# Optimization experiments

Hardware: AMD Instinct MI355X
Metric: run time of the kernel (lower is better)

Reference implementation:

```python
import jax, jax.numpy as jnp
import numpy as np

B, T, N, D = 2, 16, 512, 256
HID, HEADS = 256, 8
HD = HID // HEADS // 2  # 16
SCALE = HD ** -0.5
LAMBDA_INIT = 0.8 - 0.6 * float(np.exp(-0.3 * (2 - 1)))  # layer_idx = 2
LN_EPS = 1e-5


def setup_inputs() -> dict:
    key = jax.random.key(0)
    ks = jax.random.split(key, 8)
    return {
        "x": jax.random.normal(ks[0], (B, T, N, D), dtype=jnp.float32),
        "Wq": jax.random.normal(ks[1], (D, HID), dtype=jnp.float32) * (D ** -0.5),
        "Wk": jax.random.normal(ks[2], (D, HID), dtype=jnp.float32) * (D ** -0.5),
        "Wv": jax.random.normal(ks[3], (D, HID), dtype=jnp.float32) * (D ** -0.5),
        "lq1": jax.random.normal(ks[4], (HD,), dtype=jnp.float32) * 0.1,
        "lk1": jax.random.normal(ks[5], (HD,), dtype=jnp.float32) * 0.1,
        "lq2": jax.random.normal(ks[6], (HD,), dtype=jnp.float32) * 0.1,
        "lk2": jax.random.normal(ks[7], (HD,), dtype=jnp.float32) * 0.1,
        "ln_gamma": jnp.ones((2 * HD,), dtype=jnp.float32),
        "ln_beta": jnp.zeros((2 * HD,), dtype=jnp.float32),
    }


def _attn_pair(q, k, v1, v2):
    # q,k,v*: [BT, N, H, HD]; shared softmax applied to both value halves
    p = jax.nn.softmax(jnp.einsum('bnhd,bmhd->bhnm', q, k) * SCALE, axis=-1)
    o1 = jnp.einsum('bhnm,bmhd->bnhd', p, v1)
    o2 = jnp.einsum('bhnm,bmhd->bnhd', p, v2)
    return jnp.concatenate([o1, o2], axis=-1)  # [BT, N, H, 2*HD]


def reference(x, Wq, Wk, Wv, lq1, lk1, lq2, lk2, ln_gamma, ln_beta):
    b, t, n, d = x.shape
    # 1x1 Conv2d over channel dim == per-token linear projection
    q = jnp.einsum('btnd,dh->btnh', x, Wq).reshape(b * t, n, HEADS, 2 * HD)
    k = jnp.einsum('btnd,dh->btnh', x, Wk).reshape(b * t, n, HEADS, 2 * HD)
    v = jnp.einsum('btnd,dh->btnh', x, Wv).reshape(b * t, n, HEADS, 2 * HD)
    q1, q2 = jnp.split(q, 2, axis=-1)
    k1, k2 = jnp.split(k, 2, axis=-1)
    v1, v2 = jnp.split(v, 2, axis=-1)
    attn1 = _attn_pair(q1, k1, v1, v2)
    attn2 = _attn_pair(q2, k2, v1, v2)
    lam = jnp.exp(jnp.sum(lq1 * lk1)) - jnp.exp(jnp.sum(lq2 * lk2)) + LAMBDA_INIT
    y = attn1 - lam * attn2  # [BT, N, H, 2*HD]
    mu = jnp.mean(y, axis=-1, keepdims=True)
    var = jnp.mean(jnp.square(y - mu), axis=-1, keepdims=True)
    y = (y - mu) * jax.lax.rsqrt(var + LN_EPS) * ln_gamma + ln_beta
    y = y * (1.0 - LAMBDA_INIT)
    return y.reshape(b, t, n, HEADS * 2 * HD)
```

## Files before the change

### kernel.cpp

```cpp
#include <hip/hip_runtime.h>
#include <cmath>

typedef unsigned short u16;
typedef unsigned int   u32;
typedef __attribute__((ext_vector_type(8))) short short8;
typedef __attribute__((ext_vector_type(4))) float f32x4;

constexpr int BT    = 32;
constexpr int NTOK  = 512;
constexpr int DIM   = 256;
constexpr int HID   = 256;
constexpr int M_ROWS = BT * NTOK;
constexpr int HM     = M_ROWS * 32;
constexpr size_t TENS = (size_t)M_ROWS * HID;
constexpr float LAMBDA_INIT  = 0.35550906759096927f;
constexpr float ONE_MINUS_LI = 0.6444909324090307f;
constexpr float LN_EPS = 1e-5f;
constexpr float QSCALE = 0.36067376022224085f;

#define MFMA16(a, b, c) __builtin_amdgcn_mfma_f32_16x16x32_bf16((a), (b), (c), 0, 0, 0)

__device__ __forceinline__ u16 f2bf(float f) {
    u32 u = __float_as_uint(f);
    return (u16)((u + 0x7FFFu + ((u >> 16) & 1u)) >> 16);
}

__device__ __forceinline__ float fexp2(float x) {
#if defined(__has_builtin) && __has_builtin(__builtin_amdgcn_exp2f)
    return __builtin_amdgcn_exp2f(x);
#else
    return exp2f(x);
#endif
}

__device__ __forceinline__ u32 pack_bf16(float a, float b) {
    u32 ua = __float_as_uint(a) + 0x8000u;
    u32 ub = __float_as_uint(b) + 0x8000u;
    return __builtin_amdgcn_perm(ub, ua, 0x07060302u);
}

__global__ __launch_bounds__(256) void prep_w(const float* __restrict__ Wq,
                                              const float* __restrict__ Wk,
                                              const float* __restrict__ Wv,
                                              u16* __restrict__ Wt) {
    const float* W = (blockIdx.z == 0) ? Wq : (blockIdx.z == 1) ? Wk : Wv;
    u16* dst = Wt + (size_t)blockIdx.z * 65536;
    __shared__ float T[64][65];
    const int k0 = blockIdx.x * 64, n0 = blockIdx.y * 64;
    const int tr = threadIdx.x >> 4;
    const int tc = threadIdx.x & 15;
    #pragma unroll
    for (int i = 0; i < 4; ++i) {
        int row = tr + i * 16;
        float4 v = *(const float4*)&W[(size_t)(k0 + row) * HID + n0 + tc * 4];
        T[row][tc * 4 + 0] = v.x; T[row][tc * 4 + 1] = v.y;
        T[row][tc * 4 + 2] = v.z; T[row][tc * 4 + 3] = v.w;
    }
    __syncthreads();
    #pragma unroll
    for (int i = 0; i < 4; ++i) {
        int n = tr + i * 16;
        int k4 = tc * 4;
        uint2 pk;
        pk.x = (u32)f2bf(T[k4 + 0][n]) | ((u32)f2bf(T[k4 + 1][n]) << 16);
        pk.y = (u32)f2bf(T[k4 + 2][n]) | ((u32)f2bf(T[k4 + 3][n]) << 16);
        *(uint2*)&dst[(size_t)(n0 + n) * DIM + k0 + k4] = pk;
    }
}

__global__ __launch_bounds__(256, 3) void proj_kernel(
    const float* __restrict__ x, const u16* __restrict__ Wt,
    u16* __restrict__ Qh, u16* __restrict__ Kh, u16* __restrict__ Vh)
{
    __shared__ u16 As[64 * 72];
    __shared__ u16 Bs[3][64 * 72];

    const int tid  = threadIdx.x;
    const int m0   = blockIdx.x * 64;
    const int n0   = blockIdx.y * 64;
    const int lane = tid & 63;
    const int wv   = tid >> 6;
    const int q16  = lane & 15;
    const int quad = lane >> 4;
    const int mw   = (wv >> 1) * 32;
    const int nw   = (wv & 1) * 32;

    const int sr = tid >> 2;
    const int sc = (tid & 3) * 16;

    f32x4 acc[3][4];
    #pragma unroll
    for (int z = 0; z < 3; ++z)
        #pragma unroll
        for (int t = 0; t < 4; ++t)
            acc[z][t] = (f32x4){0.f, 0.f, 0.f, 0.f};

    for (int kk = 0; kk < DIM; kk += 64) {
        {
            const float4* xs = (const float4*)&x[(size_t)(m0 + sr) * DIM + kk + sc];
            float4 g0 = xs[0], g1 = xs[1], g2 = xs[2], g3 = xs[3];
            uint4 o0, o1;
            o0.x = (u32)f2bf(g0.x) | ((u32)f2bf(g0.y) << 16);
            o0.y = (u32)f2bf(g0.z) | ((u32)f2bf(g0.w) << 16);
            o0.z = (u32)f2bf(g1.x) | ((u32)f2bf(g1.y) << 16);
            o0.w = (u32)f2bf(g1.z) | ((u32)f2bf(g1.w) << 16);
            o1.x = (u32)f2bf(g2.x) | ((u32)f2bf(g2.y) << 16);
            o1.y = (u32)f2bf(g2.z) | ((u32)f2bf(g2.w) << 16);
            o1.z = (u32)f2bf(g3.x) | ((u32)f2bf(g3.y) << 16);
            o1.w = (u32)f2bf(g3.z) | ((u32)f2bf(g3.w) << 16);
            *(uint4*)&As[sr * 72 + sc]     = o0;
            *(uint4*)&As[sr * 72 + sc + 8] = o1;
        }
        #pragma unroll
        for (int z = 0; z < 3; ++z) {
            const uint4* ws4 = (const uint4*)&Wt[(size_t)z * 65536 + (size_t)(n0 + sr) * DIM + kk + sc];
            *(uint4*)&Bs[z][sr * 72 + sc]     = ws4[0];
            *(uint4*)&Bs[z][sr * 72 + sc + 8] = ws4[1];
        }
        __syncthreads();
        #pragma unroll
        for (int kc = 0; kc < 2; ++kc) {
            short8 a0 = *(const short8*)&As[(mw +      q16) * 72 + kc * 32 + quad * 8];
            short8 a1 = *(const short8*)&As[(mw + 16 + q16) * 72 + kc * 32 + quad * 8];
            #pragma unroll
            for (int z = 0; z < 3; ++z) {
                short8 b0 = *(const short8*)&Bs[z][(nw +      q16) * 72 + kc * 32 + quad * 8];
                short8 b1 = *(const short8*)&Bs[z][(nw + 16 + q16) * 72 + kc * 32 + quad * 8];
                acc[z][0] = MFMA16(a0, b0, acc[z][0]);
                acc[z][1] = MFMA16(a0, b1, acc[z][1]);
                acc[z][2] = MFMA16(a1, b0, acc[z][2]);
                acc[z][3] = MFMA16(a1, b1, acc[z][3]);
            }
        }
        __syncthreads();
    }

    const int hcol = (n0 + nw) >> 5;
    #pragma unroll
    for (int z = 0; z < 3; ++z) {
        u16* C = (z == 0) ? Qh : (z == 1) ? Kh : Vh;
        u16* base = C + (size_t)hcol * HM;
        const float s = (z == 0) ? QSCALE : 1.0f;
        #pragma unroll
        for (int r = 0; r < 4; ++r) {
            const int row = m0 + mw + quad * 4 + r;
            base[(size_t)row * 32 + q16]             = f2bf(acc[z][0][r] * s);
            base[(size_t)row * 32 + q16 + 16]        = f2bf(acc[z][1][r] * s);
            base[(size_t)(row + 16) * 32 + q16]      = f2bf(acc[z][2][r] * s);
            base[(size_t)(row + 16) * 32 + q16 + 16] = f2bf(acc[z][3][r] * s);
        }
    }
}

__global__ __launch_bounds__(256, 3) void attn_kernel(
    const u16* __restrict__ Qh, const u16* __restrict__ Kh, const u16* __restrict__ Vh,
    const float* __restrict__ lq1, const float* __restrict__ lk1,
    const float* __restrict__ lq2, const float* __restrict__ lk2,
    const float* __restrict__ gamma, const float* __restrict__ beta,
    float* __restrict__ out)
{
    __shared__ u16 Ks[256 * 40];
    __shared__ u16 Vts[32 * 264];
    __shared__ u16 Pbuf[4][2][16 * 40];

    const int qh  = blockIdx.x;
    const int h   = blockIdx.y;
    const int bt  = blockIdx.z;
    const int tid = threadIdx.x;
    const int lane = tid & 63;
    const int wv   = tid >> 6;
    const int q16  = lane & 15;
    const int quad = lane >> 4;

    float sa = 0.f, sb = 0.f;
    #pragma unroll
    for (int d = 0; d < 16; ++d) { sa += lq1[d] * lk1[d]; sb += lq2[d] * lk2[d]; }
    const float lam = __expf(sa) - __expf(sb) + LAMBDA_INIT;

    short8 qv[2];
    #pragma unroll
    for (int qbi = 0; qbi < 2; ++qbi) {
        const int qrow = bt * NTOK + qh * 128 + (qbi * 4 + wv) * 16 + q16;
        qv[qbi] = *(const short8*)(Qh + (size_t)h * HM + (size_t)qrow * 32 + quad * 8);
    }

    const short8 z8 = {0, 0, 0, 0, 0, 0, 0, 0};
    const f32x4  z4 = {0.f, 0.f, 0.f, 0.f};

    f32x4 o1lo[2], o1hi[2], o2lo[2], o2hi[2];
    #pragma unroll
    for (int qbi = 0; qbi < 2; ++qbi) {
        o1lo[qbi] = z4; o1hi[qbi] = z4; o2lo[qbi] = z4; o2hi[qbi] = z4;
    }
    float l1[2] = {0.f, 0.f}, l2[2] = {0.f, 0.f};

    u16* P1 = &Pbuf[wv][0][0];
    u16* P2 = &Pbuf[wv][1][0];

    for (int chunk = 0; chunk < 2; ++chunk) {
        if (chunk) __syncthreads();
        {
            const uint4* src = (const uint4*)(Kh + (size_t)h * HM +
                                (size_t)(bt * NTOK + chunk * 256 + tid) * 32);
            uint4* dst = (uint4*)&Ks[tid * 40];
            dst[0] = src[0]; dst[1] = src[1]; dst[2] = src[2]; dst[3] = src[3];
        }
        if (tid < 128) {
            const int j0 = tid * 2;
            const u16* v0 = Vh + (size_t)h * HM + (size_t)(bt * NTOK + chunk * 256 + j0) * 32;
            union U { uint4 q[4]; u32 w[16]; } ra, rb;
            #pragma unroll
            for (int i = 0; i < 4; ++i) {
                ra.q[i] = ((const uint4*)v0)[i];
                rb.q[i] = ((const uint4*)(v0 + 32))[i];
            }
            #pragma unroll
            for (int w = 0; w < 16; ++w) {
                u32 lo = __builtin_amdgcn_perm(rb.w[w], ra.w[w], 0x05040100u);
                u32 hi = __builtin_amdgcn_perm(rb.w[w], ra.w[w], 0x07060302u);
                *(u32*)&Vts[(2 * w)     * 264 + j0] = lo;
                *(u32*)&Vts[(2 * w + 1) * 264 + j0] = hi;
            }
        }
        __syncthreads();

        #pragma unroll
        for (int qbi = 0; qbi < 2; ++qbi) {
            const short8 A1 = (lane < 32) ? qv[qbi] : z8;
            const short8 A2 = (lane < 32) ? z8 : qv[qbi];
            for (int kc = 0; kc < 8; ++kc) {
                #pragma unroll
                for (int sub = 0; sub < 2; ++sub) {
                    const int key0 = kc * 32 + sub * 16;
                    short8 kf = *(const short8*)&Ks[(key0 + q16) * 40 + quad * 8];
                    f32x4 s1 = MFMA16(kf, A1, z4);
                    f32x4 s2 = MFMA16(kf, A2, z4);
                    float p0 = fexp2(s1[0]), p1 = fexp2(s1[1]);
                    float p2 = fexp2(s1[2]), p3 = fexp2(s1[3]);
                    l1[qbi] += (p0 + p1) + (p2 + p3);
                    uint2 w1; w1.x = pack_bf16(p0, p1); w1.y = pack_bf16(p2, p3);
                    *(uint2*)&P1[q16 * 40 + sub * 16 + quad * 4] = w1;
                    float r0 = fexp2(s2[0]), r1 = fexp2(s2[1]);
                    float r2 = fexp2(s2[2]), r3 = fexp2(s2[3]);
                    l2[qbi] += (r0 + r1) + (r2 + r3);
                    uint2 w2; w2.x = pack_bf16(r0, r1); w2.y = pack_bf16(r2, r3);
                    *(uint2*)&P2[q16 * 40 + sub * 16 + quad * 4] = w2;
                }
                short8 pf1 = *(const short8*)&P1[q16 * 40 + quad * 8];
                short8 pf2 = *(const short8*)&P2[q16 * 40 + quad * 8];
                short8 vlo = *(const short8*)&Vts[q16        * 264 + kc * 32 + quad * 8];
                short8 vhi = *(const short8*)&Vts[(16 + q16) * 264 + kc * 32 + quad * 8];
                o1lo[qbi] = MFMA16(pf1, vlo, o1lo[qbi]);
                o1hi[qbi] = MFMA16(pf1, vhi, o1hi[qbi]);
                o2lo[qbi] = MFMA16(pf2, vlo, o2lo[qbi]);
                o2hi[qbi] = MFMA16(pf2, vhi, o2hi[qbi]);
            }
        }
    }

    const float g_lo = gamma[q16],      g_hi = gamma[16 + q16];
    const float b_lo = beta[q16],       b_hi = beta[16 + q16];

    #pragma unroll
    for (int qbi = 0; qbi < 2; ++qbi) {
        float a = l1[qbi], b = l2[qbi];
        a += __shfl_xor(a, 16); a += __shfl_xor(a, 32);
        b += __shfl_xor(b, 16); b += __shfl_xor(b, 32);
        const float inv1 = 1.0f / a;
        const float inv2 = 1.0f / b;
        #pragma unroll
        for (int r = 0; r < 4; ++r) {
            const float i1 = __shfl(inv1, quad * 4 + r);
            const float i2 = __shfl(inv2, quad * 4 + r);
            const float ylo = o1lo[qbi][r] * i1 - lam * (o2lo[qbi][r] * i2);
            const float yhi = o1hi[qbi][r] * i1 - lam * (o2hi[qbi][r] * i2);

            float s  = ylo + yhi;
            float s2 = ylo * ylo + yhi * yhi;
            #pragma unroll
            for (int off = 1; off < 16; off <<= 1) {
                s  += __shfl_xor(s,  off);
                s2 += __shfl_xor(s2, off);
            }
            const float mu   = s * (1.0f / 32.0f);
            const float var  = s2 * (1.0f / 32.0f) - mu * mu;
            const float rstd = rsqrtf(var + LN_EPS);

            const int row = bt * NTOK + qh * 128 + (qbi * 4 + wv) * 16 + quad * 4 + r;
            float* orow = out + (size_t)row * HID + h * 32;
            orow[q16]      = ((ylo - mu) * rstd * g_lo + b_lo) * ONE_MINUS_LI;
            orow[16 + q16] = ((yhi - mu) * rstd * g_hi + b_hi) * ONE_MINUS_LI;
        }
    }
}

extern "C" void kernel_launch(void* const* d_in, const int* in_sizes, int n_in,
                              void* d_out, int out_size, void* d_ws, size_t ws_size,
                              hipStream_t stream) {
    const float* x   = (const float*)d_in[0];
    const float* Wq  = (const float*)d_in[1];
    const float* Wk  = (const float*)d_in[2];
    const float* Wv  = (const float*)d_in[3];
    const float* lq1 = (const float*)d_in[4];
    const float* lk1 = (const float*)d_in[5];
    const float* lq2 = (const float*)d_in[6];
    const float* lk2 = (const float*)d_in[7];
    const float* gam = (const float*)d_in[8];
    const float* bet = (const float*)d_in[9];
    float* out = (float*)d_out;

    u16* ws = (u16*)d_ws;
    u16* Wt = ws;
    u16* Qh = Wt + 3 * 65536;
    u16* Kh = Qh + TENS;
    u16* Vh = Kh + TENS;

    hipLaunchKernelGGL(prep_w, dim3(4, 4, 3), dim3(256), 0, stream, Wq, Wk, Wv, Wt);
    hipLaunchKernelGGL(proj_kernel, dim3(M_ROWS / 64, HID / 64), dim3(256), 0, stream,
                       x, Wt, Qh, Kh, Vh);
    hipLaunchKernelGGL(attn_kernel, dim3(4, 8, 32), dim3(256), 0, stream,
                       Qh, Kh, Vh, lq1, lk1, lq2, lk2, gam, bet, out);
}
```

Baseline: 134.3 us.

## Fuse QKV projection into attention kernel with per-(bt,head) blocks

Merges the projection and attention kernels into one kernel with one 512-thread block per (batch-time, head). Each block recomputes its head's Q/K/V from x using 32x32 MFMAs and keeps the first half of K/V in shared memory, spilling the rest to a small scratch. This removes the global round trip of the full Q/K/V tensors and one launch. In exchange x is re-read by every head (8x), the grid is only 256 blocks, and the bf16 packing now truncates instead of rounding.

```diff
diff --git a/kernel.cpp b/kernel.cpp
--- a/kernel.cpp
+++ b/kernel.cpp
@@ -3,22 +3,21 @@
 
 typedef unsigned short u16;
 typedef unsigned int   u32;
-typedef __attribute__((ext_vector_type(8))) short short8;
-typedef __attribute__((ext_vector_type(4))) float f32x4;
+typedef __attribute__((ext_vector_type(8)))  short short8;
+typedef __attribute__((ext_vector_type(4)))  float f32x4;
+typedef __attribute__((ext_vector_type(16))) float f32x16;
 
 constexpr int BT    = 32;
 constexpr int NTOK  = 512;
 constexpr int DIM   = 256;
 constexpr int HID   = 256;
-constexpr int M_ROWS = BT * NTOK;
-constexpr int HM     = M_ROWS * 32;
-constexpr size_t TENS = (size_t)M_ROWS * HID;
 constexpr float LAMBDA_INIT  = 0.35550906759096927f;
 constexpr float ONE_MINUS_LI = 0.6444909324090307f;
 constexpr float LN_EPS = 1e-5f;
 constexpr float QSCALE = 0.36067376022224085f;
 
 #define MFMA16(a, b, c) __builtin_amdgcn_mfma_f32_16x16x32_bf16((a), (b), (c), 0, 0, 0)
+#define MFMA32(a, b, c) __builtin_amdgcn_mfma_f32_32x32x16_bf16((a), (b), (c), 0, 0, 0)
 
 __device__ __forceinline__ u16 f2bf(float f) {
     u32 u = __float_as_uint(f);
@@ -33,10 +32,16 @@
 #endif
 }
 
-__device__ __forceinline__ u32 pack_bf16(float a, float b) {
-    u32 ua = __float_as_uint(a) + 0x8000u;
-    u32 ub = __float_as_uint(b) + 0x8000u;
-    return __builtin_amdgcn_perm(ub, ua, 0x07060302u);
+__device__ __forceinline__ u32 pack_trunc(float a, float b) {
+    return __builtin_amdgcn_perm(__float_as_uint(b), __float_as_uint(a), 0x07060302u);
+}
+
+__device__ __forceinline__ short8 ldb64x2(const u16* p) {
+    uint2 a = *(const uint2*)p;
+    uint2 b = *(const uint2*)(p + 4);
+    union { u32 u[4]; short8 s; } x;
+    x.u[0] = a.x; x.u[1] = a.y; x.u[2] = b.x; x.u[3] = b.y;
+    return x.s;
 }
 
 __global__ __launch_bounds__(256) void prep_w(const float* __restrict__ Wq,
@@ -68,188 +73,150 @@
     }
 }
 
-__global__ __launch_bounds__(256, 3) void proj_kernel(
+__global__ __launch_bounds__(512, 2) void fused_kernel(
     const float* __restrict__ x, const u16* __restrict__ Wt,
-    u16* __restrict__ Qh, u16* __restrict__ Kh, u16* __restrict__ Vh)
-{
-    __shared__ u16 As[64 * 72];
-    __shared__ u16 Bs[3][64 * 72];
-
-    const int tid  = threadIdx.x;
-    const int m0   = blockIdx.x * 64;
-    const int n0   = blockIdx.y * 64;
-    const int lane = tid & 63;
-    const int wv   = tid >> 6;
-    const int q16  = lane & 15;
-    const int quad = lane >> 4;
-    const int mw   = (wv >> 1) * 32;
-    const int nw   = (wv & 1) * 32;
-
-    const int sr = tid >> 2;
-    const int sc = (tid & 3) * 16;
-
-    f32x4 acc[3][4];
-    #pragma unroll
-    for (int z = 0; z < 3; ++z)
-        #pragma unroll
-        for (int t = 0; t < 4; ++t)
-            acc[z][t] = (f32x4){0.f, 0.f, 0.f, 0.f};
-
-    for (int kk = 0; kk < DIM; kk += 64) {
-        {
-            const float4* xs = (const float4*)&x[(size_t)(m0 + sr) * DIM + kk + sc];
-            float4 g0 = xs[0], g1 = xs[1], g2 = xs[2], g3 = xs[3];
-            uint4 o0, o1;
-            o0.x = (u32)f2bf(g0.x) | ((u32)f2bf(g0.y) << 16);
-            o0.y = (u32)f2bf(g0.z) | ((u32)f2bf(g0.w) << 16);
-            o0.z = (u32)f2bf(g1.x) | ((u32)f2bf(g1.y) << 16);
-            o0.w = (u32)f2bf(g1.z) | ((u32)f2bf(g1.w) << 16);
-            o1.x = (u32)f2bf(g2.x) | ((u32)f2bf(g2.y) << 16);
-            o1.y = (u32)f2bf(g2.z) | ((u32)f2bf(g2.w) << 16);
-            o1.z = (u32)f2bf(g3.x) | ((u32)f2bf(g3.y) << 16);
-            o1.w = (u32)f2bf(g3.z) | ((u32)f2bf(g3.w) << 16);
-            *(uint4*)&As[sr * 72 + sc]     = o0;
-            *(uint4*)&As[sr * 72 + sc + 8] = o1;
-        }
-        #pragma unroll
-        for (int z = 0; z < 3; ++z) {
-            const uint4* ws4 = (const uint4*)&Wt[(size_t)z * 65536 + (size_t)(n0 + sr) * DIM + kk + sc];
-            *(uint4*)&Bs[z][sr * 72 + sc]     = ws4[0];
-            *(uint4*)&Bs[z][sr * 72 + sc + 8] = ws4[1];
-        }
-        __syncthreads();
-        #pragma unroll
-        for (int kc = 0; kc < 2; ++kc) {
-            short8 a0 = *(const short8*)&As[(mw +      q16) * 72 + kc * 32 + quad * 8];
-            short8 a1 = *(const short8*)&As[(mw + 16 + q16) * 72 + kc * 32 + quad * 8];
-            #pragma unroll
-            for (int z = 0; z < 3; ++z) {
-                short8 b0 = *(const short8*)&Bs[z][(nw +      q16) * 72 + kc * 32 + quad * 8];
-                short8 b1 = *(const short8*)&Bs[z][(nw + 16 + q16) * 72 + kc * 32 + quad * 8];
-                acc[z][0] = MFMA16(a0, b0, acc[z][0]);
-                acc[z][1] = MFMA16(a0, b1, acc[z][1]);
-                acc[z][2] = MFMA16(a1, b0, acc[z][2]);
-                acc[z][3] = MFMA16(a1, b1, acc[z][3]);
-            }
-        }
-        __syncthreads();
-    }
-
-    const int hcol = (n0 + nw) >> 5;
-    #pragma unroll
-    for (int z = 0; z < 3; ++z) {
-        u16* C = (z == 0) ? Qh : (z == 1) ? Kh : Vh;
-        u16* base = C + (size_t)hcol * HM;
-        const float s = (z == 0) ? QSCALE : 1.0f;
-        #pragma unroll
-        for (int r = 0; r < 4; ++r) {
-            const int row = m0 + mw + quad * 4 + r;
-            base[(size_t)row * 32 + q16]             = f2bf(acc[z][0][r] * s);
-            base[(size_t)row * 32 + q16 + 16]        = f2bf(acc[z][1][r] * s);
-            base[(size_t)(row + 16) * 32 + q16]      = f2bf(acc[z][2][r] * s);
-            base[(size_t)(row + 16) * 32 + q16 + 16] = f2bf(acc[z][3][r] * s);
-        }
-    }
-}
-
-__global__ __launch_bounds__(256, 3) void attn_kernel(
-    const u16* __restrict__ Qh, const u16* __restrict__ Kh, const u16* __restrict__ Vh,
+    u16* __restrict__ gscratch,
     const float* __restrict__ lq1, const float* __restrict__ lk1,
     const float* __restrict__ lq2, const float* __restrict__ lk2,
     const float* __restrict__ gamma, const float* __restrict__ beta,
     float* __restrict__ out)
 {
-    __shared__ u16 Ks[256 * 40];
-    __shared__ u16 Vts[32 * 264];
-    __shared__ u16 Pbuf[4][2][16 * 40];
-
-    const int qh  = blockIdx.x;
+    __shared__ u16 KlsF[8192];
+    __shared__ u16 VtF[8192];
+    __shared__ u16 XP[10240];
+
+    const int bt  = blockIdx.x;
     const int h   = blockIdx.y;
-    const int bt  = blockIdx.z;
     const int tid = threadIdx.x;
     const int lane = tid & 63;
     const int wv   = tid >> 6;
+    const int l31  = lane & 31;
+    const int hi   = lane >> 5;
     const int q16  = lane & 15;
     const int quad = lane >> 4;
 
+    u16* gQ = gscratch + (size_t)(bt + 32 * h) * 32768;
+    u16* gK = gQ + 16384;
+    u16* gV = gK + 8192;
+
     float sa = 0.f, sb = 0.f;
     #pragma unroll
     for (int d = 0; d < 16; ++d) { sa += lq1[d] * lk1[d]; sb += lq2[d] * lk2[d]; }
     const float lam = __expf(sa) - __expf(sb) + LAMBDA_INIT;
 
-    short8 qv[2];
-    #pragma unroll
-    for (int qbi = 0; qbi < 2; ++qbi) {
-        const int qrow = bt * NTOK + qh * 128 + (qbi * 4 + wv) * 16 + q16;
-        qv[qbi] = *(const short8*)(Qh + (size_t)h * HM + (size_t)qrow * 32 + quad * 8);
-    }
-
-    const short8 z8 = {0, 0, 0, 0, 0, 0, 0, 0};
-    const f32x4  z4 = {0.f, 0.f, 0.f, 0.f};
-
-    f32x4 o1lo[2], o1hi[2], o2lo[2], o2hi[2];
-    #pragma unroll
-    for (int qbi = 0; qbi < 2; ++qbi) {
+    const f32x16 z32 = {0.f,0.f,0.f,0.f,0.f,0.f,0.f,0.f,0.f,0.f,0.f,0.f,0.f,0.f,0.f,0.f};
+
+    for (int c = 0; c < 2; ++c) {
+        f32x16 accQ = z32, accK = z32, accV = z32;
+        for (int p = 0; p < 8; ++p) {
+            __syncthreads();
+            #pragma unroll
+            for (int it = 0; it < 4; ++it) {
+                const int tok = it * 64 + wv * 8 + (lane >> 3);
+                const int cc  = (lane & 7) * 4;
+                float4 v = *(const float4*)&x[((size_t)(bt * NTOK + c * 256 + tok)) * DIM
+                                              + p * 32 + cc];
+                uint2 w;
+                w.x = (u32)f2bf(v.x) | ((u32)f2bf(v.y) << 16);
+                w.y = (u32)f2bf(v.z) | ((u32)f2bf(v.w) << 16);
+                *(uint2*)&XP[tok * 40 + cc] = w;
+            }
+            __syncthreads();
+            #pragma unroll
+            for (int ks = 0; ks < 2; ++ks) {
+                const int kg = p * 32 + ks * 16 + hi * 8;
+                short8 xf = *(const short8*)&XP[(wv * 32 + l31) * 40 + ks * 16 + hi * 8];
+                short8 wq = *(const short8*)&Wt[(size_t)0 * 65536 + (size_t)(h * 32 + l31) * DIM + kg];
+                short8 wk = *(const short8*)&Wt[(size_t)1 * 65536 + (size_t)(h * 32 + l31) * DIM + kg];
+                short8 wvv= *(const short8*)&Wt[(size_t)2 * 65536 + (size_t)(h * 32 + l31) * DIM + kg];
+                accQ = MFMA32(wq, xf, accQ);
+                accK = MFMA32(wk, xf, accK);
+                accV = MFMA32(xf, wvv, accV);
+            }
+        }
+        #pragma unroll
+        for (int rq = 0; rq < 4; ++rq) {
+            uint2 w;
+            w.x = pack_trunc(accQ[4*rq+0] * QSCALE, accQ[4*rq+1] * QSCALE);
+            w.y = pack_trunc(accQ[4*rq+2] * QSCALE, accQ[4*rq+3] * QSCALE);
+            *(uint2*)&gQ[(c * 256 + wv * 32 + l31) * 32 + 8 * rq + 4 * hi] = w;
+        }
+        #pragma unroll
+        for (int rq = 0; rq < 4; ++rq) {
+            uint2 w;
+            w.x = pack_trunc(accK[4*rq+0], accK[4*rq+1]);
+            w.y = pack_trunc(accK[4*rq+2], accK[4*rq+3]);
+            const int off = wv * 1024 + l31 * 8 + rq * 256 + 4 * hi;
+            if (c == 0) *(uint2*)&KlsF[off] = w;
+            else        *(uint2*)&gK[off]   = w;
+        }
+        #pragma unroll
+        for (int rq = 0; rq < 4; ++rq) {
+            uint2 w;
+            w.x = pack_trunc(accV[4*rq+0], accV[4*rq+1]);
+            w.y = pack_trunc(accV[4*rq+2], accV[4*rq+3]);
+            const int off = wv * 1024 + rq * 256 + l31 * 8 + 4 * hi;
+            if (c == 0) *(uint2*)&VtF[off] = w;
+            else        *(uint2*)&gV[off]  = w;
+        }
+    }
+    __syncthreads();
+
+    short8 qv[4];
+    #pragma unroll
+    for (int qbi = 0; qbi < 4; ++qbi)
+        qv[qbi] = *(const short8*)&gQ[(wv * 64 + qbi * 16 + q16) * 32 + quad * 8];
+
+    const short8 z8 = {0,0,0,0,0,0,0,0};
+    const f32x4  z4 = {0.f,0.f,0.f,0.f};
+    f32x4 o1lo[4], o1hi[4], o2lo[4], o2hi[4];
+    float l1[4] = {0.f,0.f,0.f,0.f}, l2[4] = {0.f,0.f,0.f,0.f};
+    #pragma unroll
+    for (int qbi = 0; qbi < 4; ++qbi) {
         o1lo[qbi] = z4; o1hi[qbi] = z4; o2lo[qbi] = z4; o2hi[qbi] = z4;
     }
-    float l1[2] = {0.f, 0.f}, l2[2] = {0.f, 0.f};
-
-    u16* P1 = &Pbuf[wv][0][0];
-    u16* P2 = &Pbuf[wv][1][0];
-
-    for (int chunk = 0; chunk < 2; ++chunk) {
-        if (chunk) __syncthreads();
-        {
-            const uint4* src = (const uint4*)(Kh + (size_t)h * HM +
-                                (size_t)(bt * NTOK + chunk * 256 + tid) * 32);
-            uint4* dst = (uint4*)&Ks[tid * 40];
-            dst[0] = src[0]; dst[1] = src[1]; dst[2] = src[2]; dst[3] = src[3];
-        }
-        if (tid < 128) {
-            const int j0 = tid * 2;
-            const u16* v0 = Vh + (size_t)h * HM + (size_t)(bt * NTOK + chunk * 256 + j0) * 32;
-            union U { uint4 q[4]; u32 w[16]; } ra, rb;
-            #pragma unroll
-            for (int i = 0; i < 4; ++i) {
-                ra.q[i] = ((const uint4*)v0)[i];
-                rb.q[i] = ((const uint4*)(v0 + 32))[i];
-            }
-            #pragma unroll
-            for (int w = 0; w < 16; ++w) {
-                u32 lo = __builtin_amdgcn_perm(rb.w[w], ra.w[w], 0x05040100u);
-                u32 hi = __builtin_amdgcn_perm(rb.w[w], ra.w[w], 0x07060302u);
-                *(u32*)&Vts[(2 * w)     * 264 + j0] = lo;
-                *(u32*)&Vts[(2 * w + 1) * 264 + j0] = hi;
-            }
-        }
-        __syncthreads();
-
-        #pragma unroll
-        for (int qbi = 0; qbi < 2; ++qbi) {
-            const short8 A1 = (lane < 32) ? qv[qbi] : z8;
-            const short8 A2 = (lane < 32) ? z8 : qv[qbi];
-            for (int kc = 0; kc < 8; ++kc) {
+
+    u16* P1 = &XP[wv * 1152];
+    u16* P2 = P1 + 576;
+
+    for (int kc = 0; kc < 2; ++kc) {
+        if (kc) {
+            __syncthreads();
+            #pragma unroll
+            for (int i = 0; i < 2; ++i) {
+                ((uint4*)KlsF)[tid + i * 512] = ((const uint4*)gK)[tid + i * 512];
+                ((uint4*)VtF)[tid + i * 512]  = ((const uint4*)gV)[tid + i * 512];
+            }
+            __syncthreads();
+        }
+        for (int kt = 0; kt < 8; ++kt) {
+            const short8 kf0 = *(const short8*)&KlsF[kt * 1024 + (0 * 16 + q16) * 8 + quad * 256];
+            const short8 kf1 = *(const short8*)&KlsF[kt * 1024 + (1 * 16 + q16) * 8 + quad * 256];
+            const short8 vlo = *(const short8*)&VtF[kt * 1024 + quad * 256 + q16 * 8];
+            const short8 vhi = *(const short8*)&VtF[kt * 1024 + quad * 256 + (16 + q16) * 8];
+
+            #pragma unroll
+            for (int qbi = 0; qbi < 4; ++qbi) {
+                const short8 A1 = (lane < 32) ? qv[qbi] : z8;
+                const short8 A2 = (lane < 32) ? z8 : qv[qbi];
                 #pragma unroll
                 for (int sub = 0; sub < 2; ++sub) {
-                    const int key0 = kc * 32 + sub * 16;
-                    short8 kf = *(const short8*)&Ks[(key0 + q16) * 40 + quad * 8];
+                    const short8 kf = sub ? kf1 : kf0;
                     f32x4 s1 = MFMA16(kf, A1, z4);
                     f32x4 s2 = MFMA16(kf, A2, z4);
                     float p0 = fexp2(s1[0]), p1 = fexp2(s1[1]);
                     float p2 = fexp2(s1[2]), p3 = fexp2(s1[3]);
                     l1[qbi] += (p0 + p1) + (p2 + p3);
-                    uint2 w1; w1.x = pack_bf16(p0, p1); w1.y = pack_bf16(p2, p3);
-                    *(uint2*)&P1[q16 * 40 + sub * 16 + quad * 4] = w1;
+                    uint2 w1; w1.x = pack_trunc(p0, p1); w1.y = pack_trunc(p2, p3);
+                    *(uint2*)&P1[q16 * 36 + sub * 16 + quad * 4] = w1;
                     float r0 = fexp2(s2[0]), r1 = fexp2(s2[1]);
                     float r2 = fexp2(s2[2]), r3 = fexp2(s2[3]);
                     l2[qbi] += (r0 + r1) + (r2 + r3);
-                    uint2 w2; w2.x = pack_bf16(r0, r1); w2.y = pack_bf16(r2, r3);
-                    *(uint2*)&P2[q16 * 40 + sub * 16 + quad * 4] = w2;
+                    uint2 w2; w2.x = pack_trunc(r0, r1); w2.y = pack_trunc(r2, r3);
+                    *(uint2*)&P2[q16 * 36 + sub * 16 + quad * 4] = w2;
                 }
-                short8 pf1 = *(const short8*)&P1[q16 * 40 + quad * 8];
-                short8 pf2 = *(const short8*)&P2[q16 * 40 + quad * 8];
-                short8 vlo = *(const short8*)&Vts[q16        * 264 + kc * 32 + quad * 8];
-                short8 vhi = *(const short8*)&Vts[(16 + q16) * 264 + kc * 32 + quad * 8];
+                const short8 pf1 = ldb64x2(&P1[q16 * 36 + quad * 8]);
+                const short8 pf2 = ldb64x2(&P2[q16 * 36 + quad * 8]);
                 o1lo[qbi] = MFMA16(pf1, vlo, o1lo[qbi]);
                 o1hi[qbi] = MFMA16(pf1, vhi, o1hi[qbi]);
                 o2lo[qbi] = MFMA16(pf2, vlo, o2lo[qbi]);
@@ -258,11 +225,11 @@
         }
     }
 
-    const float g_lo = gamma[q16],      g_hi = gamma[16 + q16];
-    const float b_lo = beta[q16],       b_hi = beta[16 + q16];
-
-    #pragma unroll
-    for (int qbi = 0; qbi < 2; ++qbi) {
+    const float g_lo = gamma[q16],  g_hi = gamma[16 + q16];
+    const float b_lo = beta[q16],   b_hi = beta[16 + q16];
+
+    #pragma unroll
+    for (int qbi = 0; qbi < 4; ++qbi) {
         float a = l1[qbi], b = l2[qbi];
         a += __shfl_xor(a, 16); a += __shfl_xor(a, 32);
         b += __shfl_xor(b, 16); b += __shfl_xor(b, 32);
@@ -286,7 +253,7 @@
             const float var  = s2 * (1.0f / 32.0f) - mu * mu;
             const float rstd = rsqrtf(var + LN_EPS);
 
-            const int row = bt * NTOK + qh * 128 + (qbi * 4 + wv) * 16 + quad * 4 + r;
+            const int row = bt * NTOK + wv * 64 + qbi * 16 + quad * 4 + r;
             float* orow = out + (size_t)row * HID + h * 32;
             orow[q16]      = ((ylo - mu) * rstd * g_lo + b_lo) * ONE_MINUS_LI;
             orow[16 + q16] = ((yhi - mu) * rstd * g_hi + b_hi) * ONE_MINUS_LI;
@@ -311,13 +278,9 @@
 
     u16* ws = (u16*)d_ws;
     u16* Wt = ws;
-    u16* Qh = Wt + 3 * 65536;
-    u16* Kh = Qh + TENS;
-    u16* Vh = Kh + TENS;
+    u16* gscratch = Wt + 3 * 65536;
 
     hipLaunchKernelGGL(prep_w, dim3(4, 4, 3), dim3(256), 0, stream, Wq, Wk, Wv, Wt);
-    hipLaunchKernelGGL(proj_kernel, dim3(M_ROWS / 64, HID / 64), dim3(256), 0, stream,
-                       x, Wt, Qh, Kh, Vh);
-    hipLaunchKernelGGL(attn_kernel, dim3(4, 8, 32), dim3(256), 0, stream,
-                       Qh, Kh, Vh, lq1, lk1, lq2, lk2, gam, bet, out);
-}
+    hipLaunchKernelGGL(fused_kernel, dim3(32, 8), dim3(512), 0, stream,
+                       x, Wt, gscratch, lq1, lk1, lq2, lk2, gam, bet, out);
+}
```

Measured after the change: 147.5 us. 9.8% more time.
